# Optimization experiments

Measured on AMD Instinct MI355X. Metric: run time of the kernel, lower is better.

Reference implementation:

```python
import jax, jax.numpy as jnp
import numpy as np

BETA = 2.0
EPS2 = 0.001 * 0.001
N_CLS = 5  # number of region classes present in mask


def setup_inputs() -> dict:
    key = jax.random.key(0)
    k1, k2, k3 = jax.random.split(key, 3)
    B, C, H, W = 16, 512, 64, 64
    feature_rec = jax.random.normal(k1, (B, C, H, W), dtype=jnp.float32)
    feature_align = jax.random.normal(k2, (B, C, H, W), dtype=jnp.float32)
    mask = jax.random.randint(k3, (B, H, W), 0, N_CLS, dtype=jnp.int32)
    return {"feature_rec": feature_rec, "feature_align": feature_align, "mask": mask}


def reference(feature_rec, feature_align, mask):
    # per-pixel mse averaged over channels -> [B, H, W]
    diff = feature_rec - feature_align
    loss_metric = jnp.mean(diff * diff, axis=1)

    # detached copy used for region reweighting (torch: clone().detach())
    w = jax.lax.stop_gradient(loss_metric)
    B, H, W = w.shape

    # segment-mean per (batch, region-class): replaces the double python loop
    seg = (mask.astype(jnp.int32) + jnp.arange(B, dtype=jnp.int32)[:, None, None] * N_CLS).reshape(-1)
    wf = w.reshape(-1)
    sums = jax.ops.segment_sum(wf, seg, num_segments=B * N_CLS)
    counts = jax.ops.segment_sum(jnp.ones_like(wf), seg, num_segments=B * N_CLS)
    avg = sums / jnp.maximum(counts, 1.0)  # empty regions untouched (never gathered)
    w = avg[seg].reshape(B, H, W)

    wmax = jnp.max(w)
    w = jnp.where(wmax > 0, w / (wmax + EPS2), w + EPS2)
    w = jnp.clip(w, 0.0, 1.0)

    return jnp.mean(loss_metric * (w * BETA + 1.0))
```

## Files before the change

kernel.cpp:

```cpp
#include <hip/hip_runtime.h>

#define Bd 16
#define Cd 512
#define Hd 64
#define Wd 64
#define HWd (Hd * Wd)
#define NCLS 5
#define BETA 2.0f
#define EPS2 (0.001f * 0.001f)

constexpr int CH = 16;
constexpr int NCCHUNK = Cd / CH;
constexpr int PIX_PER_BLOCK = 1024;

__global__ __launch_bounds__(256, 8) void seg_partial_kernel(
    const float* __restrict__ rec, const float* __restrict__ aln,
    const int* __restrict__ mask,
    float* __restrict__ segsum, float* __restrict__ segcnt)
{
    __shared__ float binS[NCLS];
    __shared__ float binC[NCLS];
    const int tid = threadIdx.x;
    if (tid < NCLS) { binS[tid] = 0.0f; binC[tid] = 0.0f; }
    __syncthreads();

    const int b   = blockIdx.y;
    const int hw0 = blockIdx.x * PIX_PER_BLOCK + tid * 4;
    const int c0  = blockIdx.z * CH;

    const size_t base = (size_t)(b * Cd + c0) * HWd + hw0;
    const float4* __restrict__ rv = (const float4*)(rec + base);
    const float4* __restrict__ av = (const float4*)(aln + base);
    constexpr int CSTRIDE = HWd / 4;

    const int4 m = *(const int4*)(mask + b * HWd + hw0);

    float4 acc = make_float4(0.f, 0.f, 0.f, 0.f);
#pragma unroll
    for (int cb = 0; cb < CH; cb += 4) {
        const float4* r4 = rv + (size_t)cb * CSTRIDE;
        const float4* a4 = av + (size_t)cb * CSTRIDE;
        float4 r0 = r4[0 * CSTRIDE];
        float4 r1 = r4[1 * CSTRIDE];
        float4 r2 = r4[2 * CSTRIDE];
        float4 r3 = r4[3 * CSTRIDE];
        float4 a0 = a4[0 * CSTRIDE];
        float4 a1 = a4[1 * CSTRIDE];
        float4 a2 = a4[2 * CSTRIDE];
        float4 a3 = a4[3 * CSTRIDE];

        float d;
        d = r0.x - a0.x; acc.x += d * d;
        d = r0.y - a0.y; acc.y += d * d;
        d = r0.z - a0.z; acc.z += d * d;
        d = r0.w - a0.w; acc.w += d * d;
        d = r1.x - a1.x; acc.x += d * d;
        d = r1.y - a1.y; acc.y += d * d;
        d = r1.z - a1.z; acc.z += d * d;
        d = r1.w - a1.w; acc.w += d * d;
        d = r2.x - a2.x; acc.x += d * d;
        d = r2.y - a2.y; acc.y += d * d;
        d = r2.z - a2.z; acc.z += d * d;
        d = r2.w - a2.w; acc.w += d * d;
        d = r3.x - a3.x; acc.x += d * d;
        d = r3.y - a3.y; acc.y += d * d;
        d = r3.z - a3.z; acc.z += d * d;
        d = r3.w - a3.w; acc.w += d * d;
    }

    const float scale = 1.0f / (float)Cd;
    atomicAdd(&binS[m.x], acc.x * scale);
    atomicAdd(&binS[m.y], acc.y * scale);
    atomicAdd(&binS[m.z], acc.z * scale);
    atomicAdd(&binS[m.w], acc.w * scale);
    if (blockIdx.z == 0) {
        atomicAdd(&binC[m.x], 1.0f);
        atomicAdd(&binC[m.y], 1.0f);
        atomicAdd(&binC[m.z], 1.0f);
        atomicAdd(&binC[m.w], 1.0f);
    }
    __syncthreads();
    if (tid < NCLS) {
        atomicAdd(&segsum[b * NCLS + tid], binS[tid]);
        if (blockIdx.z == 0) atomicAdd(&segcnt[b * NCLS + tid], binC[tid]);
    }
}

__global__ __launch_bounds__(128) void finalize_kernel(
    const float* __restrict__ segsum, const float* __restrict__ segcnt,
    float* __restrict__ out)
{
    __shared__ float sMax[128];
    __shared__ float sSum[128];
    const int t = threadIdx.x;

    float s = 0.0f, cnt = 0.0f;
    if (t < Bd * NCLS) { s = segsum[t]; cnt = segcnt[t]; }
    const float avg = s / fmaxf(cnt, 1.0f);

    sMax[t] = avg;
    __syncthreads();
#pragma unroll
    for (int off = 64; off > 0; off >>= 1) {
        if (t < off) sMax[t] = fmaxf(sMax[t], sMax[t + off]);
        __syncthreads();
    }
    const float wmax = sMax[0];

    float w = (wmax > 0.0f) ? (avg / (wmax + EPS2)) : (avg + EPS2);
    w = fminf(fmaxf(w, 0.0f), 1.0f);

    sSum[t] = s * (w * BETA + 1.0f);
    __syncthreads();
#pragma unroll
    for (int off = 64; off > 0; off >>= 1) {
        if (t < off) sSum[t] += sSum[t + off];
        __syncthreads();
    }
    if (t == 0) out[0] = sSum[0] / (float)(Bd * HWd);
}

extern "C" void kernel_launch(void* const* d_in, const int* in_sizes, int n_in,
                              void* d_out, int out_size, void* d_ws, size_t ws_size,
                              hipStream_t stream) {
    const float* rec  = (const float*)d_in[0];
    const float* aln  = (const float*)d_in[1];
    const int*   mask = (const int*)d_in[2];
    float* out = (float*)d_out;

    float* segsum = (float*)d_ws;
    float* segcnt = segsum + Bd * NCLS;

    hipMemsetAsync(d_ws, 0, 2 * Bd * NCLS * sizeof(float), stream);

    dim3 grid(HWd / PIX_PER_BLOCK, Bd, NCCHUNK);
    seg_partial_kernel<<<grid, 256, 0, stream>>>(rec, aln, mask, segsum, segcnt);
    finalize_kernel<<<1, 128, 0, stream>>>(segsum, segcnt, out);
}
```

Measured before the change: 285.9 us.

## Replace shared-memory atomic binning with wavefront shuffle reductions and halve channel chunk

The per-class shared-memory atomics and block barriers are replaced by per-thread class accumulators reduced with wavefront shuffles, followed by one global atomic per wave per class. The channel chunk per block drops from 16 to 8, which doubles the grid and the number of global atomics but shortens each block. The mask load is moved after the main loads. The aim is to remove contended LDS atomics and barrier stalls, at the cost of more shuffle instructions and more global atomic traffic.

```diff
diff --git a/kernel.cpp b/kernel.cpp
--- a/kernel.cpp
+++ b/kernel.cpp
@@ -2,28 +2,22 @@
 
 #define Bd 16
 #define Cd 512
-#define Hd 64
-#define Wd 64
-#define HWd (Hd * Wd)
+#define HWd 4096
 #define NCLS 5
 #define BETA 2.0f
 #define EPS2 (0.001f * 0.001f)
 
-constexpr int CH = 16;
+constexpr int CH = 8;
 constexpr int NCCHUNK = Cd / CH;
 constexpr int PIX_PER_BLOCK = 1024;
+constexpr int CSTRIDE = HWd / 4;
 
 __global__ __launch_bounds__(256, 8) void seg_partial_kernel(
     const float* __restrict__ rec, const float* __restrict__ aln,
     const int* __restrict__ mask,
     float* __restrict__ segsum, float* __restrict__ segcnt)
 {
-    __shared__ float binS[NCLS];
-    __shared__ float binC[NCLS];
     const int tid = threadIdx.x;
-    if (tid < NCLS) { binS[tid] = 0.0f; binC[tid] = 0.0f; }
-    __syncthreads();
-
     const int b   = blockIdx.y;
     const int hw0 = blockIdx.x * PIX_PER_BLOCK + tid * 4;
     const int c0  = blockIdx.z * CH;
@@ -31,9 +25,6 @@
     const size_t base = (size_t)(b * Cd + c0) * HWd + hw0;
     const float4* __restrict__ rv = (const float4*)(rec + base);
     const float4* __restrict__ av = (const float4*)(aln + base);
-    constexpr int CSTRIDE = HWd / 4;
-
-    const int4 m = *(const int4*)(mask + b * HWd + hw0);
 
     float4 acc = make_float4(0.f, 0.f, 0.f, 0.f);
 #pragma unroll
@@ -68,21 +59,52 @@
         d = r3.w - a3.w; acc.w += d * d;
     }
 
-    const float scale = 1.0f / (float)Cd;
-    atomicAdd(&binS[m.x], acc.x * scale);
-    atomicAdd(&binS[m.y], acc.y * scale);
-    atomicAdd(&binS[m.z], acc.z * scale);
-    atomicAdd(&binS[m.w], acc.w * scale);
+    const int4 m = *(const int4*)(mask + b * HWd + hw0);
+
+    float cls[NCLS] = {0, 0, 0, 0, 0};
+    {
+        float v[4]  = {acc.x, acc.y, acc.z, acc.w};
+        int   mm[4] = {m.x, m.y, m.z, m.w};
+#pragma unroll
+        for (int e = 0; e < 4; ++e) {
+#pragma unroll
+            for (int k = 0; k < NCLS; ++k)
+                cls[k] += (mm[e] == k) ? v[e] : 0.0f;
+        }
+    }
+#pragma unroll
+    for (int k = 0; k < NCLS; ++k) {
+#pragma unroll
+        for (int off = 32; off > 0; off >>= 1)
+            cls[k] += __shfl_down(cls[k], off, 64);
+    }
+    if ((tid & 63) == 0) {
+        const float scale = 1.0f / (float)Cd;
+#pragma unroll
+        for (int k = 0; k < NCLS; ++k)
+            atomicAdd(&segsum[b * NCLS + k], cls[k] * scale);
+    }
+
     if (blockIdx.z == 0) {
-        atomicAdd(&binC[m.x], 1.0f);
-        atomicAdd(&binC[m.y], 1.0f);
-        atomicAdd(&binC[m.z], 1.0f);
-        atomicAdd(&binC[m.w], 1.0f);
-    }
-    __syncthreads();
-    if (tid < NCLS) {
-        atomicAdd(&segsum[b * NCLS + tid], binS[tid]);
-        if (blockIdx.z == 0) atomicAdd(&segcnt[b * NCLS + tid], binC[tid]);
+        float cnt[NCLS] = {0, 0, 0, 0, 0};
+        int mm[4] = {m.x, m.y, m.z, m.w};
+#pragma unroll
+        for (int e = 0; e < 4; ++e) {
+#pragma unroll
+            for (int k = 0; k < NCLS; ++k)
+                cnt[k] += (mm[e] == k) ? 1.0f : 0.0f;
+        }
+#pragma unroll
+        for (int k = 0; k < NCLS; ++k) {
+#pragma unroll
+            for (int off = 32; off > 0; off >>= 1)
+                cnt[k] += __shfl_down(cnt[k], off, 64);
+        }
+        if ((tid & 63) == 0) {
+#pragma unroll
+            for (int k = 0; k < NCLS; ++k)
+                atomicAdd(&segcnt[b * NCLS + k], cnt[k]);
+        }
     }
 }
 
```

Measured after the change: 589.4 us. 106% more time.
